# Performance work log

Hardware: AMD Instinct MI355X
Metric: run time of the kernel (lower is better)

The kernel has to match this reference:

```python
import jax, jax.numpy as jnp
import numpy as np

RADIUS = 0.1          # acceptance_radius
CONF = 0.2            # confidence_threshold
MIN_LOCAL = 3         # min_local_correspondences
MIN_GLOBAL = 256      # min_global_correspondences
STEPS = 5             # num_refinement_steps
EPS = 1e-5
NTH = 8               # candidate thresholds CONF - 0.05*k (replaces data-dependent while loop)


def weighted_procrustes(src, tgt, w):
    """Weighted Kabsch. src/tgt: (..., N, 3), w: (..., N). Returns R (...,3,3), t (...,3)."""
    w = w / (jnp.sum(w, axis=-1, keepdims=True) + EPS)
    src_c = jnp.einsum('...n,...nc->...c', w, src)
    tgt_c = jnp.einsum('...n,...nc->...c', w, tgt)
    s0 = src - src_c[..., None, :]
    t0 = tgt - tgt_c[..., None, :]
    H = jnp.einsum('...nc,...n,...nd->...cd', s0, w, t0)  # (...,3,3)
    U, S, Vt = jnp.linalg.svd(H)
    V = jnp.swapaxes(Vt, -1, -2)
    det = jnp.linalg.det(jnp.matmul(V, jnp.swapaxes(U, -1, -2)))
    d = jnp.stack([jnp.ones_like(det), jnp.ones_like(det), det], axis=-1)
    R = jnp.einsum('...ik,...k,...jk->...ij', V, d, U)
    t = tgt_c - jnp.einsum('...ij,...j->...i', R, src_c)
    return R, t


def setup_inputs() -> dict:
    key = jax.random.key(0)
    k0, k1, k2 = jax.random.split(key, 3)
    B, K = 128, 64
    src = jax.random.normal(k0, (B, K, 3), dtype=jnp.float32)
    tgt = jax.random.normal(k1, (B, K, 3), dtype=jnp.float32)
    score_mat = jax.random.normal(k2, (B, K, K), dtype=jnp.float32) * 2.0 - 4.0
    src_masks = jnp.ones((B, K), dtype=bool)
    tgt_masks = jnp.ones((B, K), dtype=bool)
    return {
        'src_knn_points': src,
        'tgt_knn_points': tgt,
        'src_knn_masks': src_masks,
        'tgt_knn_masks': tgt_masks,
        'score_mat': score_mat,
    }


def reference(src_knn_points, tgt_knn_points, src_knn_masks, tgt_knn_masks, score_mat):
    B, K, _ = score_mat.shape
    score = jax.nn.sigmoid(score_mat)
    mask = src_knn_masks[:, :, None] & tgt_knn_masks[:, None, :]  # (B,K,K)

    # --- threshold search (dense replacement for the while loop) ---
    mg = jnp.minimum(min(3 * K, MIN_GLOBAL), jnp.sum(mask))
    th = CONF - 0.05 * jnp.arange(NTH, dtype=score.dtype)
    cnts = jnp.sum((score[None] > th[:, None, None, None]) & mask[None], axis=(1, 2, 3))
    thr = th[jnp.argmax(cnts >= mg)]  # first threshold with enough correspondences

    corr = (score > thr) & mask          # dense corr_mat (B,K,K)
    score = score * corr.astype(score.dtype)

    # --- dense (masked) correspondence batching: all (i,j) pairs per patch ---
    srcP = jnp.broadcast_to(src_knn_points[:, :, None, :], (B, K, K, 3)).reshape(B, K * K, 3)
    tgtP = jnp.broadcast_to(tgt_knn_points[:, None, :, :], (B, K, K, 3)).reshape(B, K * K, 3)
    w = score.reshape(B, K * K)

    # per-patch hypothesis transforms (zero-weight pairs are ignored by Procrustes)
    Rb, tb = weighted_procrustes(srcP, tgtP, w)  # (B,3,3), (B,3)
    counts_b = jnp.sum(corr, axis=(1, 2))
    valid = counts_b >= MIN_LOCAL

    # --- hypothesis verification: inlier counts over all global correspondences ---
    aligned = jnp.einsum('bxy,piy->bpix', Rb, src_knn_points) + tb[:, None, None, :]  # (B,B,K,3)
    cross = jnp.einsum('bpix,pjx->bpij', aligned, tgt_knn_points)                     # (B,B,K,K)
    res2 = (jnp.sum(aligned ** 2, -1)[..., None]
            + jnp.sum(tgt_knn_points ** 2, -1)[None, :, None, :]
            - 2.0 * cross)
    inlier = (res2 < RADIUS ** 2) & corr[None]                                        # (B,B,K,K)
    cnt_T = jnp.where(valid, jnp.sum(inlier, axis=(1, 2, 3)), -1)
    best = jnp.argmax(cnt_T)

    cur = score * inlier[best].astype(score.dtype)

    # --- global refinement ---
    src_all = srcP.reshape(-1, 3)
    tgt_all = tgtP.reshape(-1, 3)
    score_all = score.reshape(-1)
    R, t = weighted_procrustes(src_all, tgt_all, cur.reshape(-1))
    for _ in range(STEPS - 1):
        res = jnp.linalg.norm(tgt_all - (src_all @ R.T + t), axis=-1)
        cur_all = score_all * (res < RADIUS).astype(score.dtype)
        R, t = weighted_procrustes(src_all, tgt_all, cur_all)

    estimated_transform = jnp.eye(4, dtype=score.dtype).at[:3, :3].set(R).at[:3, 3].set(t)
    return estimated_transform, score  # score = dense-masked correspondence scores (B,K,K)
```

## Files before the change

### kernel.cpp

```cpp
#include <hip/hip_runtime.h>
#include <math.h>

#define BB   128
#define KK   64
#define K2   (KK*KK)
#define NTH  8
#define MG   192
#define MIN_LOCAL 3
#define RADIUS2 0.01f
#define RADIUSF 0.1f
#define GRID 256
#define TPB  512
#define NW   8
#define AGT  __HIP_MEMORY_SCOPE_AGENT

static constexpr size_t OFF_ARR   = 0;
static constexpr size_t OFF_MAIL  = 4096;
static constexpr size_t ZERO_BYTES= 8192;
static constexpr size_t OFF_CNT8S = 8192;
static constexpr size_t OFF_CNTB  = 12288;
static constexpr size_t OFF_MSLOT = 28672;
static constexpr size_t OFF_VALID = 45056;
static constexpr size_t OFF_RB    = 45568;
static constexpr size_t OFF_CB    = 51712;

__device__ inline void mail_wait(int* mail, int blk, int ep) {
    int spins = 0;
    unsigned long long t0 = 0;
    while (__hip_atomic_load(&mail[blk * 4], __ATOMIC_RELAXED, AGT) < ep) {
        __builtin_amdgcn_s_sleep(2);
        if ((++spins & 63) == 0) {
            unsigned long long now = __builtin_amdgcn_s_memrealtime();
            if (t0 == 0) t0 = now;
            else if (now - t0 > 10000000ULL) break;
        }
    }
    __atomic_signal_fence(__ATOMIC_SEQ_CST);
}

__device__ inline void sync_point(int* arrived, int* mail, int blk, int lane, int wave,
                                  int ep, int nparts) {
    __syncthreads();
    if (blk == 0) {
        if (wave == 0) {
            if (lane == 0)
                __hip_atomic_store(&arrived[0], ep, __ATOMIC_RELEASE, AGT);
            int spins = 0;
            unsigned long long t0 = 0;
            for (;;) {
                bool ok = true;
                for (int i = lane; i < nparts; i += 64)
                    ok &= (__hip_atomic_load(&arrived[i * 4], __ATOMIC_RELAXED, AGT) >= ep);
                if (__ballot(ok) == ~0ULL) break;
                __builtin_amdgcn_s_sleep(1);
                if ((++spins & 31) == 0) {
                    unsigned long long now = __builtin_amdgcn_s_memrealtime();
                    if (t0 == 0) t0 = now;
                    else if (now - t0 > 10000000ULL) break;
                }
            }
            for (int i = lane; i < GRID; i += 64)
                __hip_atomic_store(&mail[i * 4], ep, __ATOMIC_RELAXED, AGT);
        }
    } else {
        if (lane == 0 && wave == 0) {
            __hip_atomic_store(&arrived[blk * 4], ep, __ATOMIC_RELEASE, AGT);
            mail_wait(mail, blk, ep);
        }
    }
    __atomic_signal_fence(__ATOMIC_SEQ_CST);
    __syncthreads();
}

__device__ inline void eigvec3(const double A[3][3], double lambda, double v[3]) {
    double r0x = A[0][0] - lambda, r0y = A[0][1], r0z = A[0][2];
    double r1x = A[0][1], r1y = A[1][1] - lambda, r1z = A[1][2];
    double r2x = A[0][2], r2y = A[1][2], r2z = A[2][2] - lambda;
    double c0x = r0y * r1z - r0z * r1y, c0y = r0z * r1x - r0x * r1z, c0z = r0x * r1y - r0y * r1x;
    double c1x = r0y * r2z - r0z * r2y, c1y = r0z * r2x - r0x * r2z, c1z = r0x * r2y - r0y * r2x;
    double c2x = r1y * r2z - r1z * r2y, c2y = r1z * r2x - r1x * r2z, c2z = r1x * r2y - r1y * r2x;
    double n0 = c0x * c0x + c0y * c0y + c0z * c0z;
    double n1 = c1x * c1x + c1y * c1y + c1z * c1z;
    double n2 = c2x * c2x + c2y * c2y + c2z * c2z;
    double bx = c0x, by = c0y, bz = c0z, nb = n0;
    if (n1 > nb) { bx = c1x; by = c1y; bz = c1z; nb = n1; }
    if (n2 > nb) { bx = c2x; by = c2y; bz = c2z; nb = n2; }
    if (nb < 1e-280) { v[0] = 1.0; v[1] = 0.0; v[2] = 0.0; return; }
    double s = 1.0 / sqrt(nb);
    v[0] = bx * s; v[1] = by * s; v[2] = bz * s;
}

__device__ inline void eig3(const double A[3][3], double V[3][3], double lam[3]) {
    double q = (A[0][0] + A[1][1] + A[2][2]) / 3.0;
    double a00 = A[0][0] - q, a11 = A[1][1] - q, a22 = A[2][2] - q;
    double p1 = A[0][1] * A[0][1] + A[0][2] * A[0][2] + A[1][2] * A[1][2];
    double p2 = a00 * a00 + a11 * a11 + a22 * a22 + 2.0 * p1;
    if (p2 < 1e-280) {
        lam[0] = q; lam[1] = q; lam[2] = q;
        for (int i = 0; i < 3; i++)
            for (int j = 0; j < 3; j++) V[i][j] = (i == j) ? 1.0 : 0.0;
        return;
    }
    double p = sqrt(p2 / 6.0);
    double ip = 1.0 / p;
    double b00 = a00 * ip, b11 = a11 * ip, b22 = a22 * ip;
    double b01 = A[0][1] * ip, b02 = A[0][2] * ip, b12 = A[1][2] * ip;
    double detB = b00 * (b11 * b22 - b12 * b12)
                - b01 * (b01 * b22 - b12 * b02)
                + b02 * (b01 * b12 - b11 * b02);
    double r = 0.5 * detB;
    r = fmin(1.0, fmax(-1.0, r));
    double phi = acos(r) / 3.0;
    double l0 = q + 2.0 * p * cos(phi);
    double l2 = q + 2.0 * p * cos(phi + 2.0943951023931953);
    double l1 = 3.0 * q - l0 - l2;
    lam[0] = l0; lam[1] = l1; lam[2] = l2;

    double v0[3], v2[3];
    eigvec3(A, l0, v0);
    eigvec3(A, l2, v2);
    double d = v0[0] * v2[0] + v0[1] * v2[1] + v0[2] * v2[2];
    v2[0] -= d * v0[0]; v2[1] -= d * v0[1]; v2[2] -= d * v0[2];
    double n = v2[0] * v2[0] + v2[1] * v2[1] + v2[2] * v2[2];
    if (n < 1e-280) {
        int k = (fabs(v0[0]) <= fabs(v0[1]) && fabs(v0[0]) <= fabs(v0[2])) ? 0
              : ((fabs(v0[1]) <= fabs(v0[2])) ? 1 : 2);
        double ax[3] = {0.0, 0.0, 0.0}; ax[k] = 1.0;
        double dd = v0[k];
        v2[0] = ax[0] - dd * v0[0]; v2[1] = ax[1] - dd * v0[1]; v2[2] = ax[2] - dd * v0[2];
        n = v2[0] * v2[0] + v2[1] * v2[1] + v2[2] * v2[2];
    }
    double s2 = 1.0 / sqrt(n);
    v2[0] *= s2; v2[1] *= s2; v2[2] *= s2;
    double v1[3] = { v2[1] * v0[2] - v2[2] * v0[1],
                     v2[2] * v0[0] - v2[0] * v0[2],
                     v2[0] * v0[1] - v2[1] * v0[0] };
    for (int i = 0; i < 3; i++) { V[i][0] = v0[i]; V[i][1] = v1[i]; V[i][2] = v2[i]; }
}

__device__ inline void kabsch_from_moments(const double* m, double R[3][3], double t[3]) {
    double W = m[0];
    double denom = W + 1e-5;
    double s = W / denom;
    double sc[3], tc[3];
    for (int c = 0; c < 3; c++) { sc[c] = m[1 + c] / denom; tc[c] = m[4 + c] / denom; }
    double H[3][3];
    for (int c = 0; c < 3; c++)
        for (int d = 0; d < 3; d++)
            H[c][d] = m[7 + c * 3 + d] / denom - (2.0 - s) * sc[c] * tc[d];
    double B3[3][3];
    for (int i = 0; i < 3; i++)
        for (int j = 0; j < 3; j++) {
            double v = 0.0;
            for (int k = 0; k < 3; k++) v += H[k][i] * H[k][j];
            B3[i][j] = v;
        }
    double V[3][3], lam[3];
    eig3(B3, V, lam);
    double inv[3];
    for (int k = 0; k < 3; k++) {
        double sg = sqrt(fmax(lam[k], 0.0));
        inv[k] = (sg > 1e-150) ? 1.0 / sg : 0.0;
    }
    double detH = H[0][0] * (H[1][1] * H[2][2] - H[1][2] * H[2][1])
                - H[0][1] * (H[1][0] * H[2][2] - H[1][2] * H[2][0])
                + H[0][2] * (H[1][0] * H[2][1] - H[1][1] * H[2][0]);
    if (detH < 0.0) inv[2] = -inv[2];
    double T2[3][3];
    for (int i = 0; i < 3; i++)
        for (int j = 0; j < 3; j++) {
            double v = 0.0;
            for (int k = 0; k < 3; k++) v += V[i][k] * inv[k] * V[j][k];
            T2[i][j] = v;
        }
    for (int i = 0; i < 3; i++)
        for (int j = 0; j < 3; j++) {
            double v = 0.0;
            for (int k = 0; k < 3; k++) v += T2[i][k] * H[j][k];
            R[i][j] = v;
        }
    for (int i = 0; i < 3; i++) {
        double v = tc[i];
        for (int j = 0; j < 3; j++) v -= R[i][j] * sc[j];
        t[i] = v;
    }
}

__global__ __launch_bounds__(TPB) void k_all(
    const float* __restrict__ src, const float* __restrict__ tgt,
    const float* __restrict__ sm, float* __restrict__ out, char* __restrict__ ws)
{
    int* arrived  = (int*)(ws + OFF_ARR);
    int* mail     = (int*)(ws + OFF_MAIL);
    int* cnt8s    = (int*)(ws + OFF_CNT8S);
    unsigned int* cntB = (unsigned int*)(ws + OFF_CNTB);
    float* mslot  = (float*)(ws + OFF_MSLOT);
    int* validA   = (int*)(ws + OFF_VALID);
    float* Rb     = (float*)(ws + OFF_RB);
    unsigned long long* corrb = (unsigned long long*)(ws + OFF_CB);
    float* score  = out + 16;

    const int t = threadIdx.x, lane = t & 63, wave = t >> 6;
    const int blk = blockIdx.x;

    __shared__ float sScore[4096];
    __shared__ float sS[192];
    __shared__ float sT[256];
    __shared__ float sAl[256];
    __shared__ float sRTall[384];
    __shared__ unsigned long long sCB[64];
    __shared__ float sRed[NW * 16];
    __shared__ int sRedi[NW];
    __shared__ int sCnt[32];
    __shared__ int sC8[NTH];
    __shared__ int sCT[BB], sVv[BB];
    __shared__ int sCTp[512];
    __shared__ double sPartD[512];
    __shared__ double sM[16];
    __shared__ double sRTd[12];
    __shared__ float sRTf[12];
    __shared__ int sBest;
    __shared__ float sThr;

    if (blk < BB) {
        int b = blk;
        float xv[8];
        #pragma unroll
        for (int u = 0; u < 8; u++)
            xv[u] = sm[b * K2 + (u * NW + wave) * KK + lane];
        if (t < 192) sS[t] = src[b * 192 + t];
        if (t < 64) {
            float x = tgt[b * 192 + t * 3], y = tgt[b * 192 + t * 3 + 1], z = tgt[b * 192 + t * 3 + 2];
            sT[t * 4] = x; sT[t * 4 + 1] = y; sT[t * 4 + 2] = z; sT[t * 4 + 3] = x * x + y * y + z * z;
        }
        if (t < NTH) sC8[t] = 0;
        __syncthreads();
        int ck[NTH];
        #pragma unroll
        for (int k = 0; k < NTH; k++) ck[k] = 0;
        for (int u = 0; u < 8; u++) {
            int i = u * NW + wave;
            float s = 1.0f / (1.0f + expf(-xv[u]));
            sScore[i * KK + lane] = s;
            #pragma unroll
            for (int k = 0; k < NTH; k++) {
                unsigned long long bal = __ballot(s > (0.2f - 0.05f * (float)k));
                ck[k] += (int)__popcll(bal);
            }
        }
        if (lane == 0) {
            #pragma unroll
            for (int k = 0; k < NTH; k++) atomicAdd(&sC8[k], ck[k]);
        }
        __syncthreads();
        if (t < NTH)
            __hip_atomic_store(&cnt8s[blk * NTH + t], sC8[t], __ATOMIC_RELAXED, AGT);
        sync_point(arrived, mail, blk, lane, wave, 1, BB);

        if (wave == 0) {
            int k = lane & 7, c = lane >> 3;
            int sct = 0;
            for (int j = 0; j < 16; j++)
                sct += __hip_atomic_load(&cnt8s[(c * 16 + j) * NTH + k], __ATOMIC_RELAXED, AGT);
            sct += __shfl_down(sct, 32);
            sct += __shfl_down(sct, 16);
            sct += __shfl_down(sct, 8);
            unsigned long long bal = __ballot(lane < 8 && sct >= MG);
            if (lane == 0) {
                int kk2 = bal ? (int)__builtin_ctzll(bal) : 0;
                sThr = 0.2f - 0.05f * (float)kk2;
            }
        }
        __syncthreads();

        float thr = sThr;
        float tx0 = sT[lane * 4], ty0 = sT[lane * 4 + 1], tz0 = sT[lane * 4 + 2];
        float acc[16];
        #pragma unroll
        for (int k = 0; k < 16; k++) acc[k] = 0.0f;
        int cnt = 0;
        for (int u = 0; u < 8; u++) {
            int i = u * NW + wave;
            float s = sScore[i * KK + lane];
            bool c = (s > thr);
            float w = c ? s : 0.0f;
            score[b * K2 + i * KK + lane] = w;
            unsigned long long bal = __ballot(c);
            if (lane == 0)
                __hip_atomic_store(&corrb[b * KK + i], bal, __ATOMIC_RELAXED, AGT);
            cnt += c ? 1 : 0;
            float sx = sS[i * 3], sy = sS[i * 3 + 1], sz = sS[i * 3 + 2];
            acc[0]  += w;
            acc[1]  += w * sx; acc[2]  += w * sy; acc[3]  += w * sz;
            acc[4]  += w * tx0; acc[5]  += w * ty0; acc[6]  += w * tz0;
            acc[7]  += w * sx * tx0; acc[8]  += w * sx * ty0; acc[9]  += w * sx * tz0;
            acc[10] += w * sy * tx0; acc[11] += w * sy * ty0; acc[12] += w * sy * tz0;
            acc[13] += w * sz * tx0; acc[14] += w * sz * ty0; acc[15] += w * sz * tz0;
        }
        #pragma unroll
        for (int off = 32; off; off >>= 1) {
            #pragma unroll
            for (int k = 0; k < 16; k++) acc[k] += __shfl_down(acc[k], off);
            cnt += __shfl_down(cnt, off);
        }
        if (lane == 0) {
            for (int k = 0; k < 16; k++) sRed[wave * 16 + k] = acc[k];
            sRedi[wave] = cnt;
        }
        __syncthreads();
        if (t == 0) {
            double m[16];
            for (int k = 0; k < 16; k++) {
                float v = 0.0f;
                for (int wv = 0; wv < NW; wv++) v += sRed[wv * 16 + k];
                m[k] = (double)v;
            }
            double R[3][3], tv[3];
            kabsch_from_moments(m, R, tv);
            for (int i = 0; i < 3; i++)
                for (int j = 0; j < 3; j++)
                    __hip_atomic_store(&Rb[b * 12 + i * 3 + j], (float)R[i][j], __ATOMIC_RELAXED, AGT);
            for (int i = 0; i < 3; i++)
                __hip_atomic_store(&Rb[b * 12 + 9 + i], (float)tv[i], __ATOMIC_RELAXED, AGT);
            int ctot = 0;
            for (int wv = 0; wv < NW; wv++) ctot += sRedi[wv];
            __hip_atomic_store(&validA[b], (ctot >= MIN_LOCAL) ? 1 : 0, __ATOMIC_RELAXED, AGT);
        }
        sync_point(arrived, mail, blk, lane, wave, 2, BB);
    } else {
        if (t == 0) mail_wait(mail, blk, 2);
        __syncthreads();
    }

    if (t < 32) sCnt[t] = 0;
    for (int u = 0; u < 2; u++) {
        int unit = blk + u * GRID;
        int p = unit >> 2, g4 = unit & 3, b0 = g4 * 32;
        __syncthreads();
        if (t < 192) sS[t] = src[p * 192 + t];
        if (t < 64) {
            float x = tgt[p * 192 + t * 3], y = tgt[p * 192 + t * 3 + 1], z = tgt[p * 192 + t * 3 + 2];
            sT[t * 4] = x; sT[t * 4 + 1] = y; sT[t * 4 + 2] = z; sT[t * 4 + 3] = x * x + y * y + z * z;
            sCB[t] = __hip_atomic_load(&corrb[p * KK + t], __ATOMIC_RELAXED, AGT);
        }
        if (t < 384)
            sRTall[t] = __hip_atomic_load(&Rb[b0 * 12 + t], __ATOMIC_RELAXED, AGT);
        __syncthreads();

        int i = t >> 3, jg = t & 7;
        float sx = sS[i * 3], sy = sS[i * 3 + 1], sz = sS[i * 3 + 2];
        unsigned int m8 = (unsigned int)((sCB[i] >> (jg * 8)) & 0xFFULL);
        const float4* sT4 = (const float4*)sT;
        float4 tv0 = sT4[jg * 8 + 0], tv1 = sT4[jg * 8 + 1];
        float4 tv2 = sT4[jg * 8 + 2], tv3 = sT4[jg * 8 + 3];
        float4 tv4 = sT4[jg * 8 + 4], tv5 = sT4[jg * 8 + 5];
        float4 tv6 = sT4[jg * 8 + 6], tv7 = sT4[jg * 8 + 7];

        for (int h = 0; h < 32; h++) {
            const float* RT = &sRTall[h * 12];
            float ax = RT[0] * sx + RT[1] * sy + RT[2] * sz + RT[9];
            float ay = RT[3] * sx + RT[4] * sy + RT[5] * sz + RT[10];
            float az = RT[6] * sx + RT[7] * sy + RT[8] * sz + RT[11];
            float sa = ax * ax + ay * ay + az * az;
            int c = 0;
            #define VCHK(TV, JJ) { \
                float d2 = (sa + TV.w) - 2.0f * (ax * TV.x + ay * TV.y + az * TV.z); \
                c += (d2 < RADIUS2 && ((m8 >> JJ) & 1u)) ? 1 : 0; }
            VCHK(tv0, 0) VCHK(tv1, 1) VCHK(tv2, 2) VCHK(tv3, 3)
            VCHK(tv4, 4) VCHK(tv5, 5) VCHK(tv6, 6) VCHK(tv7, 7)
            #undef VCHK
            #pragma unroll
            for (int off = 32; off; off >>= 1) c += __shfl_down(c, off);
            if (lane == 0) atomicAdd(&sCnt[h], c);
        }
    }
    __syncthreads();
    if (t < 16) {
        unsigned int pk = ((unsigned int)sCnt[2 * t] & 0xFFFFu)
                        | ((unsigned int)sCnt[2 * t + 1] << 16);
        __hip_atomic_store(&cntB[blk * 16 + t], pk, __ATOMIC_RELAXED, AGT);
    }
    if (blk >= BB) {
        __syncthreads();
        if (t == 0) __hip_atomic_store(&arrived[blk * 4], 3, __ATOMIC_RELEASE, AGT);
        return;
    }
    sync_point(arrived, mail, blk, lane, wave, 3, GRID);

    {
        int p = blk;
        if (t < 192) sS[t] = src[p * 192 + t];
        if (t < 64) {
            float x = tgt[p * 192 + t * 3], y = tgt[p * 192 + t * 3 + 1], z = tgt[p * 192 + t * 3 + 2];
            sT[t * 4] = x; sT[t * 4 + 1] = y; sT[t * 4 + 2] = z; sT[t * 4 + 3] = x * x + y * y + z * z;
        }
    }
    {
        int q = t >> 7, h = t & 127;
        int g = h >> 5, r = h & 31, w = r >> 1, sh = (r & 1) * 16;
        int ssum = 0;
        for (int m = q * 16; m < q * 16 + 16; m++) {
            unsigned int wv = __hip_atomic_load(&cntB[((4 * m + g) << 4) + w],
                                                __ATOMIC_RELAXED, AGT);
            ssum += (int)((wv >> sh) & 0xFFFFu);
        }
        sCTp[t] = ssum;
    }
    __syncthreads();
    if (t < BB) {
        sCT[t] = sCTp[t] + sCTp[t + 128] + sCTp[t + 256] + sCTp[t + 384];
        sVv[t] = __hip_atomic_load(&validA[t], __ATOMIC_RELAXED, AGT);
    }
    __syncthreads();
    if (t == 0) {
        int best = 0, bc = -2;
        for (int b = 0; b < BB; b++) {
            int c = sVv[b] ? sCT[b] : -1;
            if (c > bc) { bc = c; best = b; }
        }
        sBest = best;
    }
    __syncthreads();
    if (t < 12)
        sRTd[t] = (double)__hip_atomic_load(&Rb[sBest * 12 + t], __ATOMIC_RELAXED, AGT);
    __syncthreads();

    float thr = sThr;
    for (int it = 0; it < 5; it++) {
        if (t < 12) sRTf[t] = (float)sRTd[t];
        __syncthreads();
        if (t < 64) {
            float x = sS[t * 3], y = sS[t * 3 + 1], z = sS[t * 3 + 2];
            float ax = sRTf[0] * x + sRTf[1] * y + sRTf[2] * z + sRTf[9];
            float ay = sRTf[3] * x + sRTf[4] * y + sRTf[5] * z + sRTf[10];
            float az = sRTf[6] * x + sRTf[7] * y + sRTf[8] * z + sRTf[11];
            sAl[t * 4] = ax; sAl[t * 4 + 1] = ay; sAl[t * 4 + 2] = az;
            sAl[t * 4 + 3] = ax * ax + ay * ay + az * az;
        }
        __syncthreads();
        float tx = sT[lane * 4], ty = sT[lane * 4 + 1], tz = sT[lane * 4 + 2], st2 = sT[lane * 4 + 3];
        float acc[16];
        #pragma unroll
        for (int k = 0; k < 16; k++) acc[k] = 0.0f;
        for (int u = 0; u < 8; u++) {
            int i = u * NW + wave;
            float sx = sS[i * 3], sy = sS[i * 3 + 1], sz = sS[i * 3 + 2];
            float ax = sAl[i * 4], ay = sAl[i * 4 + 1], az = sAl[i * 4 + 2], sa = sAl[i * 4 + 3];
            bool pred;
            if (it == 0) {
                float d2 = (sa + st2) - 2.0f * (ax * tx + ay * ty + az * tz);
                pred = (d2 < RADIUS2);
            } else {
                float dx = tx - ax, dy = ty - ay, dz = tz - az;
                pred = (sqrtf(dx * dx + dy * dy + dz * dz) < RADIUSF);
            }
            float s = sScore[i * KK + lane];
            float w = (s > thr) ? s : 0.0f;
            float wf = pred ? w : 0.0f;
            acc[0]  += wf;
            acc[1]  += wf * sx; acc[2]  += wf * sy; acc[3]  += wf * sz;
            acc[4]  += wf * tx; acc[5]  += wf * ty; acc[6]  += wf * tz;
            acc[7]  += wf * sx * tx; acc[8]  += wf * sx * ty; acc[9]  += wf * sx * tz;
            acc[10] += wf * sy * tx; acc[11] += wf * sy * ty; acc[12] += wf * sy * tz;
            acc[13] += wf * sz * tx; acc[14] += wf * sz * ty; acc[15] += wf * sz * tz;
        }
        #pragma unroll
        for (int off = 32; off; off >>= 1)
            #pragma unroll
            for (int k = 0; k < 16; k++) acc[k] += __shfl_down(acc[k], off);
        if (lane == 0)
            for (int k = 0; k < 16; k++) sRed[wave * 16 + k] = acc[k];
        __syncthreads();
        if (t < 16) {
            float v = 0.0f;
            for (int wv = 0; wv < NW; wv++) v += sRed[wv * 16 + t];
            __hip_atomic_store(&mslot[(((it & 1) * BB + blk) << 4) + t], v,
                               __ATOMIC_RELAXED, AGT);
        }
        if (it < 4) {
            sync_point(arrived, mail, blk, lane, wave, 4 + it, BB);
            {
                int k = t & 15, c = t >> 4;
                double sd = 0.0;
                for (int j = 0; j < 4; j++)
                    sd += (double)__hip_atomic_load(
                        &mslot[(((it & 1) * BB + c * 4 + j) << 4) + k],
                        __ATOMIC_RELAXED, AGT);
                sPartD[t] = sd;
            }
            __syncthreads();
            if (t < 16) {
                double md = 0.0;
                for (int c = 0; c < 32; c++) md += sPartD[c * 16 + t];
                sM[t] = md;
            }
            __syncthreads();
            if (t == 0) {
                double m[16];
                for (int k = 0; k < 16; k++) m[k] = sM[k];
                double R[3][3], tv[3];
                kabsch_from_moments(m, R, tv);
                for (int i = 0; i < 3; i++)
                    for (int j = 0; j < 3; j++) sRTd[i * 3 + j] = R[i][j];
                for (int i = 0; i < 3; i++) sRTd[9 + i] = tv[i];
            }
            __syncthreads();
        } else {
            __syncthreads();
            if (blk != 0) {
                if (t == 0) __hip_atomic_store(&arrived[blk * 4], 8, __ATOMIC_RELEASE, AGT);
                return;
            }
            if (wave == 0) {
                if (lane == 0) __hip_atomic_store(&arrived[0], 8, __ATOMIC_RELEASE, AGT);
                int spins = 0;
                unsigned long long t0 = 0;
                for (;;) {
                    bool ok = true;
                    for (int i = lane; i < BB; i += 64)
                        ok &= (__hip_atomic_load(&arrived[i * 4], __ATOMIC_RELAXED, AGT) >= 8);
                    if (__ballot(ok) == ~0ULL) break;
                    __builtin_amdgcn_s_sleep(1);
                    if ((++spins & 31) == 0) {
                        unsigned long long now = __builtin_amdgcn_s_memrealtime();
                        if (t0 == 0) t0 = now;
                        else if (now - t0 > 10000000ULL) break;
                    }
                }
            }
            __atomic_signal_fence(__ATOMIC_SEQ_CST);
            __syncthreads();
            {
                int k = t & 15, c = t >> 4;
                double sd = 0.0;
                for (int j = 0; j < 4; j++)
                    sd += (double)__hip_atomic_load(&mslot[((c * 4 + j) << 4) + k],
                                                    __ATOMIC_RELAXED, AGT);
                sPartD[t] = sd;
            }
            __syncthreads();
            if (t < 16) {
                double md = 0.0;
                for (int c = 0; c < 32; c++) md += sPartD[c * 16 + t];
                sM[t] = md;
            }
            __syncthreads();
            if (t == 0) {
                double m[16];
                for (int k = 0; k < 16; k++) m[k] = sM[k];
                double R[3][3], tv[3];
                kabsch_from_moments(m, R, tv);
                for (int i = 0; i < 3; i++) {
                    for (int j = 0; j < 3; j++) out[i * 4 + j] = (float)R[i][j];
                    out[i * 4 + 3] = (float)tv[i];
                }
                out[12] = 0.0f; out[13] = 0.0f; out[14] = 0.0f; out[15] = 1.0f;
            }
        }
    }
}

extern "C" void kernel_launch(void* const* d_in, const int* in_sizes, int n_in,
                              void* d_out, int out_size, void* d_ws, size_t ws_size,
                              hipStream_t stream) {
    const float* src = (const float*)d_in[0];
    const float* tgt = (const float*)d_in[1];
    const float* sm  = (const float*)d_in[4];
    float* out = (float*)d_out;
    char* ws = (char*)d_ws;

    hipMemsetAsync(d_ws, 0, ZERO_BYTES, stream);

    k_all<<<GRID, TPB, 0, stream>>>(src, tgt, sm, out, ws);
}
```

Before: 176.9 us.

## Replace grid barriers with per-block tags and single-block reduce-and-publish

Swaps the centralized arrive/mailbox grid barrier for per-block ready tags. Block 0 alone reduces the partial results (threshold counts, best-hypothesis counts, moments), solves Kabsch, and publishes the answer through a small mailbox that the other blocks poll. The verification stage now waits only on the 32 hypothesis blocks and 2 point blocks it actually depends on, instead of the whole grid. This is meant to cut barrier round-trips and the redundant per-block reductions. In exchange, rotation values are published as float rather than double, and the spin loops poll more aggressively.

```diff
diff --git a/kernel.cpp b/kernel.cpp
--- a/kernel.cpp
+++ b/kernel.cpp
@@ -14,21 +14,31 @@
 #define NW   8
 #define AGT  __HIP_MEMORY_SCOPE_AGENT
 
-static constexpr size_t OFF_ARR   = 0;
-static constexpr size_t OFF_MAIL  = 4096;
-static constexpr size_t ZERO_BYTES= 8192;
-static constexpr size_t OFF_CNT8S = 8192;
-static constexpr size_t OFF_CNTB  = 12288;
-static constexpr size_t OFF_MSLOT = 28672;
-static constexpr size_t OFF_VALID = 45056;
-static constexpr size_t OFF_RB    = 45568;
-static constexpr size_t OFF_CB    = 51712;
-
-__device__ inline void mail_wait(int* mail, int blk, int ep) {
+static constexpr size_t OFF_TAGA  = 0;
+static constexpr size_t OFF_TAGB  = 512;
+static constexpr size_t OFF_TAGC  = 1024;
+static constexpr size_t OFF_TAGM  = 2048;
+static constexpr size_t OFF_PUB   = 3072;
+static constexpr size_t ZERO_BYTES= 3328;
+static constexpr size_t OFF_CNT8S = 4096;
+static constexpr size_t OFF_CNTB  = 8192;
+static constexpr size_t OFF_MSLOT = 24576;
+static constexpr size_t OFF_VALID = 40960;
+static constexpr size_t OFF_RB    = 41472;
+static constexpr size_t OFF_CB    = 47616;
+
+#define PUB_THR_TAG 0
+#define PUB_THR_VAL 1
+#define PUB_BEST_TAG 16
+#define PUB_BEST_VAL 17
+#define PUB_R0 32
+#define PUB_R1 48
+
+__device__ inline void wait_ge(int* p, int val) {
     int spins = 0;
     unsigned long long t0 = 0;
-    while (__hip_atomic_load(&mail[blk * 4], __ATOMIC_RELAXED, AGT) < ep) {
-        __builtin_amdgcn_s_sleep(2);
+    while (__hip_atomic_load(p, __ATOMIC_RELAXED, AGT) < val) {
+        if (spins > 8) __builtin_amdgcn_s_sleep(2);
         if ((++spins & 63) == 0) {
             unsigned long long now = __builtin_amdgcn_s_memrealtime();
             if (t0 == 0) t0 = now;
@@ -38,38 +48,61 @@
     __atomic_signal_fence(__ATOMIC_SEQ_CST);
 }
 
-__device__ inline void sync_point(int* arrived, int* mail, int blk, int lane, int wave,
-                                  int ep, int nparts) {
-    __syncthreads();
-    if (blk == 0) {
-        if (wave == 0) {
-            if (lane == 0)
-                __hip_atomic_store(&arrived[0], ep, __ATOMIC_RELEASE, AGT);
-            int spins = 0;
-            unsigned long long t0 = 0;
-            for (;;) {
-                bool ok = true;
-                for (int i = lane; i < nparts; i += 64)
-                    ok &= (__hip_atomic_load(&arrived[i * 4], __ATOMIC_RELAXED, AGT) >= ep);
-                if (__ballot(ok) == ~0ULL) break;
-                __builtin_amdgcn_s_sleep(1);
-                if ((++spins & 31) == 0) {
-                    unsigned long long now = __builtin_amdgcn_s_memrealtime();
-                    if (t0 == 0) t0 = now;
-                    else if (now - t0 > 10000000ULL) break;
-                }
-            }
-            for (int i = lane; i < GRID; i += 64)
-                __hip_atomic_store(&mail[i * 4], ep, __ATOMIC_RELAXED, AGT);
-        }
-    } else {
-        if (lane == 0 && wave == 0) {
-            __hip_atomic_store(&arrived[blk * 4], ep, __ATOMIC_RELEASE, AGT);
-            mail_wait(mail, blk, ep);
+__device__ inline void wait128(const int* tags, int lane, int val) {
+    int spins = 0;
+    unsigned long long t0 = 0;
+    for (;;) {
+        bool ok = (__hip_atomic_load(&tags[lane],      __ATOMIC_RELAXED, AGT) >= val)
+               && (__hip_atomic_load(&tags[lane + 64], __ATOMIC_RELAXED, AGT) >= val);
+        if (__ballot(ok) == ~0ULL) break;
+        if (spins > 16) __builtin_amdgcn_s_sleep(1);
+        if ((++spins & 63) == 0) {
+            unsigned long long now = __builtin_amdgcn_s_memrealtime();
+            if (t0 == 0) t0 = now;
+            else if (__ballot(now - t0 > 10000000ULL) != 0ULL) break;
         }
     }
     __atomic_signal_fence(__ATOMIC_SEQ_CST);
-    __syncthreads();
+}
+
+__device__ inline void wait256(const int* tags, int lane, int val) {
+    int spins = 0;
+    unsigned long long t0 = 0;
+    for (;;) {
+        bool ok = true;
+        #pragma unroll
+        for (int j = 0; j < 4; j++)
+            ok &= (__hip_atomic_load(&tags[lane + j * 64], __ATOMIC_RELAXED, AGT) >= val);
+        if (__ballot(ok) == ~0ULL) break;
+        if (spins > 16) __builtin_amdgcn_s_sleep(1);
+        if ((++spins & 63) == 0) {
+            unsigned long long now = __builtin_amdgcn_s_memrealtime();
+            if (t0 == 0) t0 = now;
+            else if (__ballot(now - t0 > 10000000ULL) != 0ULL) break;
+        }
+    }
+    __atomic_signal_fence(__ATOMIC_SEQ_CST);
+}
+
+__device__ inline void wait_set34(const int* tagB, int lane, int b0, int p0, int p1) {
+    int idx = -1;
+    if (lane < 32) idx = b0 + lane;
+    else if (lane == 32) idx = p0;
+    else if (lane == 33) idx = p1;
+    int spins = 0;
+    unsigned long long t0 = 0;
+    for (;;) {
+        bool ok = (idx < 0) ||
+                  (__hip_atomic_load(&tagB[idx], __ATOMIC_RELAXED, AGT) >= 1);
+        if (__ballot(ok) == ~0ULL) break;
+        if (spins > 8) __builtin_amdgcn_s_sleep(8);
+        if ((++spins & 63) == 0) {
+            unsigned long long now = __builtin_amdgcn_s_memrealtime();
+            if (t0 == 0) t0 = now;
+            else if (__ballot(now - t0 > 10000000ULL) != 0ULL) break;
+        }
+    }
+    __atomic_signal_fence(__ATOMIC_SEQ_CST);
 }
 
 __device__ inline void eigvec3(const double A[3][3], double lambda, double v[3]) {
@@ -190,8 +223,11 @@
     const float* __restrict__ src, const float* __restrict__ tgt,
     const float* __restrict__ sm, float* __restrict__ out, char* __restrict__ ws)
 {
-    int* arrived  = (int*)(ws + OFF_ARR);
-    int* mail     = (int*)(ws + OFF_MAIL);
+    int* tagA     = (int*)(ws + OFF_TAGA);
+    int* tagB     = (int*)(ws + OFF_TAGB);
+    int* tagC     = (int*)(ws + OFF_TAGC);
+    int* tagM     = (int*)(ws + OFF_TAGM);
+    int* pub      = (int*)(ws + OFF_PUB);
     int* cnt8s    = (int*)(ws + OFF_CNT8S);
     unsigned int* cntB = (unsigned int*)(ws + OFF_CNTB);
     float* mslot  = (float*)(ws + OFF_MSLOT);
@@ -215,8 +251,6 @@
     __shared__ int sC8[NTH];
     __shared__ int sCT[BB], sVv[BB];
     __shared__ int sCTp[512];
-    __shared__ double sPartD[512];
-    __shared__ double sM[16];
     __shared__ double sRTd[12];
     __shared__ float sRTf[12];
     __shared__ int sBest;
@@ -255,23 +289,41 @@
         __syncthreads();
         if (t < NTH)
             __hip_atomic_store(&cnt8s[blk * NTH + t], sC8[t], __ATOMIC_RELAXED, AGT);
-        sync_point(arrived, mail, blk, lane, wave, 1, BB);
-
-        if (wave == 0) {
-            int k = lane & 7, c = lane >> 3;
-            int sct = 0;
-            for (int j = 0; j < 16; j++)
-                sct += __hip_atomic_load(&cnt8s[(c * 16 + j) * NTH + k], __ATOMIC_RELAXED, AGT);
-            sct += __shfl_down(sct, 32);
-            sct += __shfl_down(sct, 16);
-            sct += __shfl_down(sct, 8);
-            unsigned long long bal = __ballot(lane < 8 && sct >= MG);
-            if (lane == 0) {
-                int kk2 = bal ? (int)__builtin_ctzll(bal) : 0;
-                sThr = 0.2f - 0.05f * (float)kk2;
-            }
-        }
-        __syncthreads();
+        __syncthreads();
+        if (t == 0)
+            __hip_atomic_store(&tagA[blk], 1, __ATOMIC_RELEASE, AGT);
+
+        if (blk == 0) {
+            if (wave == 0) {
+                wait128(tagA, lane, 1);
+                int a[NTH];
+                #pragma unroll
+                for (int k = 0; k < NTH; k++)
+                    a[k] = __hip_atomic_load(&cnt8s[lane * NTH + k], __ATOMIC_RELAXED, AGT)
+                         + __hip_atomic_load(&cnt8s[(lane + 64) * NTH + k], __ATOMIC_RELAXED, AGT);
+                #pragma unroll
+                for (int off = 32; off; off >>= 1)
+                    #pragma unroll
+                    for (int k = 0; k < NTH; k++) a[k] += __shfl_down(a[k], off);
+                if (lane == 0) {
+                    int kk2 = 0; bool found = false;
+                    #pragma unroll
+                    for (int k = 0; k < NTH; k++)
+                        if (!found && a[k] >= MG) { kk2 = k; found = true; }
+                    float thr = 0.2f - 0.05f * (float)kk2;
+                    __hip_atomic_store(&pub[PUB_THR_VAL], __float_as_int(thr), __ATOMIC_RELAXED, AGT);
+                    __hip_atomic_store(&pub[PUB_THR_TAG], 1, __ATOMIC_RELEASE, AGT);
+                    sThr = thr;
+                }
+            }
+            __syncthreads();
+        } else {
+            if (t == 0) {
+                wait_ge(&pub[PUB_THR_TAG], 1);
+                sThr = __int_as_float(__hip_atomic_load(&pub[PUB_THR_VAL], __ATOMIC_RELAXED, AGT));
+            }
+            __syncthreads();
+        }
 
         float thr = sThr;
         float tx0 = sT[lane * 4], ty0 = sT[lane * 4 + 1], tz0 = sT[lane * 4 + 2];
@@ -326,52 +378,54 @@
             for (int wv = 0; wv < NW; wv++) ctot += sRedi[wv];
             __hip_atomic_store(&validA[b], (ctot >= MIN_LOCAL) ? 1 : 0, __ATOMIC_RELAXED, AGT);
         }
-        sync_point(arrived, mail, blk, lane, wave, 2, BB);
-    } else {
-        if (t == 0) mail_wait(mail, blk, 2);
-        __syncthreads();
-    }
-
-    if (t < 32) sCnt[t] = 0;
-    for (int u = 0; u < 2; u++) {
-        int unit = blk + u * GRID;
-        int p = unit >> 2, g4 = unit & 3, b0 = g4 * 32;
-        __syncthreads();
-        if (t < 192) sS[t] = src[p * 192 + t];
-        if (t < 64) {
-            float x = tgt[p * 192 + t * 3], y = tgt[p * 192 + t * 3 + 1], z = tgt[p * 192 + t * 3 + 2];
-            sT[t * 4] = x; sT[t * 4 + 1] = y; sT[t * 4 + 2] = z; sT[t * 4 + 3] = x * x + y * y + z * z;
-            sCB[t] = __hip_atomic_load(&corrb[p * KK + t], __ATOMIC_RELAXED, AGT);
-        }
-        if (t < 384)
-            sRTall[t] = __hip_atomic_load(&Rb[b0 * 12 + t], __ATOMIC_RELAXED, AGT);
-        __syncthreads();
-
-        int i = t >> 3, jg = t & 7;
-        float sx = sS[i * 3], sy = sS[i * 3 + 1], sz = sS[i * 3 + 2];
-        unsigned int m8 = (unsigned int)((sCB[i] >> (jg * 8)) & 0xFFULL);
-        const float4* sT4 = (const float4*)sT;
-        float4 tv0 = sT4[jg * 8 + 0], tv1 = sT4[jg * 8 + 1];
-        float4 tv2 = sT4[jg * 8 + 2], tv3 = sT4[jg * 8 + 3];
-        float4 tv4 = sT4[jg * 8 + 4], tv5 = sT4[jg * 8 + 5];
-        float4 tv6 = sT4[jg * 8 + 6], tv7 = sT4[jg * 8 + 7];
-
-        for (int h = 0; h < 32; h++) {
-            const float* RT = &sRTall[h * 12];
-            float ax = RT[0] * sx + RT[1] * sy + RT[2] * sz + RT[9];
-            float ay = RT[3] * sx + RT[4] * sy + RT[5] * sz + RT[10];
-            float az = RT[6] * sx + RT[7] * sy + RT[8] * sz + RT[11];
-            float sa = ax * ax + ay * ay + az * az;
-            int c = 0;
-            #define VCHK(TV, JJ) { \
-                float d2 = (sa + TV.w) - 2.0f * (ax * TV.x + ay * TV.y + az * TV.z); \
-                c += (d2 < RADIUS2 && ((m8 >> JJ) & 1u)) ? 1 : 0; }
-            VCHK(tv0, 0) VCHK(tv1, 1) VCHK(tv2, 2) VCHK(tv3, 3)
-            VCHK(tv4, 4) VCHK(tv5, 5) VCHK(tv6, 6) VCHK(tv7, 7)
-            #undef VCHK
-            #pragma unroll
-            for (int off = 32; off; off >>= 1) c += __shfl_down(c, off);
-            if (lane == 0) atomicAdd(&sCnt[h], c);
+        __syncthreads();
+        if (t == 0)
+            __hip_atomic_store(&tagB[blk], 1, __ATOMIC_RELEASE, AGT);
+    }
+
+    {
+        int p0 = blk >> 2, b0 = (blk & 3) * 32;
+        if (wave == 0) wait_set34(tagB, lane, b0, p0, p0 + 64);
+        if (t < 32) sCnt[t] = 0;
+        for (int u = 0; u < 2; u++) {
+            int p = p0 + u * 64;
+            __syncthreads();
+            if (t < 192) sS[t] = src[p * 192 + t];
+            if (t < 64) {
+                float x = tgt[p * 192 + t * 3], y = tgt[p * 192 + t * 3 + 1], z = tgt[p * 192 + t * 3 + 2];
+                sT[t * 4] = x; sT[t * 4 + 1] = y; sT[t * 4 + 2] = z; sT[t * 4 + 3] = x * x + y * y + z * z;
+                sCB[t] = __hip_atomic_load(&corrb[p * KK + t], __ATOMIC_RELAXED, AGT);
+            }
+            if (t < 384)
+                sRTall[t] = __hip_atomic_load(&Rb[b0 * 12 + t], __ATOMIC_RELAXED, AGT);
+            __syncthreads();
+
+            int i = t >> 3, jg = t & 7;
+            float sx = sS[i * 3], sy = sS[i * 3 + 1], sz = sS[i * 3 + 2];
+            unsigned int m8 = (unsigned int)((sCB[i] >> (jg * 8)) & 0xFFULL);
+            const float4* sT4 = (const float4*)sT;
+            float4 tv0 = sT4[jg * 8 + 0], tv1 = sT4[jg * 8 + 1];
+            float4 tv2 = sT4[jg * 8 + 2], tv3 = sT4[jg * 8 + 3];
+            float4 tv4 = sT4[jg * 8 + 4], tv5 = sT4[jg * 8 + 5];
+            float4 tv6 = sT4[jg * 8 + 6], tv7 = sT4[jg * 8 + 7];
+
+            for (int h = 0; h < 32; h++) {
+                const float* RT = &sRTall[h * 12];
+                float ax = RT[0] * sx + RT[1] * sy + RT[2] * sz + RT[9];
+                float ay = RT[3] * sx + RT[4] * sy + RT[5] * sz + RT[10];
+                float az = RT[6] * sx + RT[7] * sy + RT[8] * sz + RT[11];
+                float sa = ax * ax + ay * ay + az * az;
+                int c = 0;
+                #define VCHK(TV, JJ) { \
+                    float d2 = (sa + TV.w) - 2.0f * (ax * TV.x + ay * TV.y + az * TV.z); \
+                    c += (d2 < RADIUS2 && ((m8 >> JJ) & 1u)) ? 1 : 0; }
+                VCHK(tv0, 0) VCHK(tv1, 1) VCHK(tv2, 2) VCHK(tv3, 3)
+                VCHK(tv4, 4) VCHK(tv5, 5) VCHK(tv6, 6) VCHK(tv7, 7)
+                #undef VCHK
+                #pragma unroll
+                for (int off = 32; off; off >>= 1) c += __shfl_down(c, off);
+                if (lane == 0) atomicAdd(&sCnt[h], c);
+            }
         }
     }
     __syncthreads();
@@ -380,47 +434,54 @@
                         | ((unsigned int)sCnt[2 * t + 1] << 16);
         __hip_atomic_store(&cntB[blk * 16 + t], pk, __ATOMIC_RELAXED, AGT);
     }
-    if (blk >= BB) {
-        __syncthreads();
-        if (t == 0) __hip_atomic_store(&arrived[blk * 4], 3, __ATOMIC_RELEASE, AGT);
-        return;
-    }
-    sync_point(arrived, mail, blk, lane, wave, 3, GRID);
-
-    {
-        int p = blk;
-        if (t < 192) sS[t] = src[p * 192 + t];
-        if (t < 64) {
-            float x = tgt[p * 192 + t * 3], y = tgt[p * 192 + t * 3 + 1], z = tgt[p * 192 + t * 3 + 2];
-            sT[t * 4] = x; sT[t * 4 + 1] = y; sT[t * 4 + 2] = z; sT[t * 4 + 3] = x * x + y * y + z * z;
-        }
-    }
-    {
-        int q = t >> 7, h = t & 127;
-        int g = h >> 5, r = h & 31, w = r >> 1, sh = (r & 1) * 16;
-        int ssum = 0;
-        for (int m = q * 16; m < q * 16 + 16; m++) {
-            unsigned int wv = __hip_atomic_load(&cntB[((4 * m + g) << 4) + w],
-                                                __ATOMIC_RELAXED, AGT);
-            ssum += (int)((wv >> sh) & 0xFFFFu);
-        }
-        sCTp[t] = ssum;
-    }
     __syncthreads();
-    if (t < BB) {
-        sCT[t] = sCTp[t] + sCTp[t + 128] + sCTp[t + 256] + sCTp[t + 384];
-        sVv[t] = __hip_atomic_load(&validA[t], __ATOMIC_RELAXED, AGT);
-    }
-    __syncthreads();
-    if (t == 0) {
-        int best = 0, bc = -2;
-        for (int b = 0; b < BB; b++) {
-            int c = sVv[b] ? sCT[b] : -1;
-            if (c > bc) { bc = c; best = b; }
-        }
-        sBest = best;
-    }
-    __syncthreads();
+    if (t == 0)
+        __hip_atomic_store(&tagC[blk], 1, __ATOMIC_RELEASE, AGT);
+    if (blk >= BB) return;
+
+    if (t < 192) sS[t] = src[blk * 192 + t];
+    if (t < 64) {
+        float x = tgt[blk * 192 + t * 3], y = tgt[blk * 192 + t * 3 + 1], z = tgt[blk * 192 + t * 3 + 2];
+        sT[t * 4] = x; sT[t * 4 + 1] = y; sT[t * 4 + 2] = z; sT[t * 4 + 3] = x * x + y * y + z * z;
+    }
+    if (blk == 0) {
+        if (wave == 0) wait256(tagC, lane, 1);
+        __syncthreads();
+        {
+            int q = t >> 7, h = t & 127;
+            int g = h >> 5, r = h & 31, w = r >> 1, sh = (r & 1) * 16;
+            int ssum = 0;
+            for (int m = q * 16; m < q * 16 + 16; m++) {
+                unsigned int wv = __hip_atomic_load(&cntB[((4 * m + g) << 4) + w],
+                                                    __ATOMIC_RELAXED, AGT);
+                ssum += (int)((wv >> sh) & 0xFFFFu);
+            }
+            sCTp[t] = ssum;
+        }
+        __syncthreads();
+        if (t < BB) {
+            sCT[t] = sCTp[t] + sCTp[t + 128] + sCTp[t + 256] + sCTp[t + 384];
+            sVv[t] = __hip_atomic_load(&validA[t], __ATOMIC_RELAXED, AGT);
+        }
+        __syncthreads();
+        if (t == 0) {
+            int best = 0, bc = -2;
+            for (int b = 0; b < BB; b++) {
+                int c = sVv[b] ? sCT[b] : -1;
+                if (c > bc) { bc = c; best = b; }
+            }
+            __hip_atomic_store(&pub[PUB_BEST_VAL], best, __ATOMIC_RELAXED, AGT);
+            __hip_atomic_store(&pub[PUB_BEST_TAG], 1, __ATOMIC_RELEASE, AGT);
+            sBest = best;
+        }
+        __syncthreads();
+    } else {
+        if (t == 0) {
+            wait_ge(&pub[PUB_BEST_TAG], 1);
+            sBest = __hip_atomic_load(&pub[PUB_BEST_VAL], __ATOMIC_RELAXED, AGT);
+        }
+        __syncthreads();
+    }
     if (t < 12)
         sRTd[t] = (double)__hip_atomic_load(&Rb[sBest * 12 + t], __ATOMIC_RELAXED, AGT);
     __syncthreads();
@@ -477,85 +538,78 @@
             __hip_atomic_store(&mslot[(((it & 1) * BB + blk) << 4) + t], v,
                                __ATOMIC_RELAXED, AGT);
         }
+        __syncthreads();
+        if (t == 0)
+            __hip_atomic_store(&tagM[(it & 1) * BB + blk], it + 1, __ATOMIC_RELEASE, AGT);
+
         if (it < 4) {
-            sync_point(arrived, mail, blk, lane, wave, 4 + it, BB);
-            {
-                int k = t & 15, c = t >> 4;
-                double sd = 0.0;
-                for (int j = 0; j < 4; j++)
-                    sd += (double)__hip_atomic_load(
-                        &mslot[(((it & 1) * BB + c * 4 + j) << 4) + k],
-                        __ATOMIC_RELAXED, AGT);
-                sPartD[t] = sd;
-            }
-            __syncthreads();
-            if (t < 16) {
-                double md = 0.0;
-                for (int c = 0; c < 32; c++) md += sPartD[c * 16 + t];
-                sM[t] = md;
-            }
-            __syncthreads();
-            if (t == 0) {
-                double m[16];
-                for (int k = 0; k < 16; k++) m[k] = sM[k];
-                double R[3][3], tv[3];
-                kabsch_from_moments(m, R, tv);
-                for (int i = 0; i < 3; i++)
-                    for (int j = 0; j < 3; j++) sRTd[i * 3 + j] = R[i][j];
-                for (int i = 0; i < 3; i++) sRTd[9 + i] = tv[i];
-            }
-            __syncthreads();
-        } else {
-            __syncthreads();
-            if (blk != 0) {
-                if (t == 0) __hip_atomic_store(&arrived[blk * 4], 8, __ATOMIC_RELEASE, AGT);
-                return;
-            }
-            if (wave == 0) {
-                if (lane == 0) __hip_atomic_store(&arrived[0], 8, __ATOMIC_RELEASE, AGT);
-                int spins = 0;
-                unsigned long long t0 = 0;
-                for (;;) {
-                    bool ok = true;
-                    for (int i = lane; i < BB; i += 64)
-                        ok &= (__hip_atomic_load(&arrived[i * 4], __ATOMIC_RELAXED, AGT) >= 8);
-                    if (__ballot(ok) == ~0ULL) break;
-                    __builtin_amdgcn_s_sleep(1);
-                    if ((++spins & 31) == 0) {
-                        unsigned long long now = __builtin_amdgcn_s_memrealtime();
-                        if (t0 == 0) t0 = now;
-                        else if (now - t0 > 10000000ULL) break;
+            int base = (it & 1) ? PUB_R1 : PUB_R0;
+            if (blk == 0) {
+                if (wave == 0) {
+                    wait128(&tagM[(it & 1) * BB], lane, it + 1);
+                    double a[16];
+                    #pragma unroll
+                    for (int k = 0; k < 16; k++)
+                        a[k] = (double)__hip_atomic_load(
+                                   &mslot[(((it & 1) * BB + lane) << 4) + k], __ATOMIC_RELAXED, AGT)
+                             + (double)__hip_atomic_load(
+                                   &mslot[(((it & 1) * BB + lane + 64) << 4) + k], __ATOMIC_RELAXED, AGT);
+                    #pragma unroll
+                    for (int off = 32; off; off >>= 1)
+                        #pragma unroll
+                        for (int k = 0; k < 16; k++) a[k] += __shfl_down(a[k], off);
+                    if (lane == 0) {
+                        double R[3][3], tv[3];
+                        kabsch_from_moments(a, R, tv);
+                        for (int i = 0; i < 3; i++)
+                            for (int j = 0; j < 3; j++) sRTd[i * 3 + j] = R[i][j];
+                        for (int i = 0; i < 3; i++) sRTd[9 + i] = tv[i];
+                        #pragma unroll
+                        for (int i = 0; i < 3; i++)
+                            for (int j = 0; j < 3; j++)
+                                __hip_atomic_store(&pub[base + 1 + i * 3 + j],
+                                    __float_as_int((float)R[i][j]), __ATOMIC_RELAXED, AGT);
+                        #pragma unroll
+                        for (int i = 0; i < 3; i++)
+                            __hip_atomic_store(&pub[base + 10 + i],
+                                __float_as_int((float)tv[i]), __ATOMIC_RELAXED, AGT);
+                        __hip_atomic_store(&pub[base], it + 1, __ATOMIC_RELEASE, AGT);
                     }
                 }
-            }
-            __atomic_signal_fence(__ATOMIC_SEQ_CST);
-            __syncthreads();
-            {
-                int k = t & 15, c = t >> 4;
-                double sd = 0.0;
-                for (int j = 0; j < 4; j++)
-                    sd += (double)__hip_atomic_load(&mslot[((c * 4 + j) << 4) + k],
-                                                    __ATOMIC_RELAXED, AGT);
-                sPartD[t] = sd;
-            }
-            __syncthreads();
-            if (t < 16) {
-                double md = 0.0;
-                for (int c = 0; c < 32; c++) md += sPartD[c * 16 + t];
-                sM[t] = md;
-            }
-            __syncthreads();
-            if (t == 0) {
-                double m[16];
-                for (int k = 0; k < 16; k++) m[k] = sM[k];
-                double R[3][3], tv[3];
-                kabsch_from_moments(m, R, tv);
-                for (int i = 0; i < 3; i++) {
-                    for (int j = 0; j < 3; j++) out[i * 4 + j] = (float)R[i][j];
-                    out[i * 4 + 3] = (float)tv[i];
+                __syncthreads();
+            } else {
+                if (t == 0) {
+                    wait_ge(&pub[base], it + 1);
+                    for (int i = 0; i < 12; i++)
+                        sRTd[i] = (double)__int_as_float(
+                            __hip_atomic_load(&pub[base + 1 + i], __ATOMIC_RELAXED, AGT));
                 }
-                out[12] = 0.0f; out[13] = 0.0f; out[14] = 0.0f; out[15] = 1.0f;
-            }
+                __syncthreads();
+            }
+        } else {
+            if (blk != 0) return;
+            if (wave == 0) {
+                wait128(&tagM[0], lane, 5);
+                double a[16];
+                #pragma unroll
+                for (int k = 0; k < 16; k++)
+                    a[k] = (double)__hip_atomic_load(&mslot[(lane << 4) + k], __ATOMIC_RELAXED, AGT)
+                         + (double)__hip_atomic_load(&mslot[((lane + 64) << 4) + k], __ATOMIC_RELAXED, AGT);
+                #pragma unroll
+                for (int off = 32; off; off >>= 1)
+                    #pragma unroll
+                    for (int k = 0; k < 16; k++) a[k] += __shfl_down(a[k], off);
+                if (lane == 0) {
+                    double R[3][3], tv[3];
+                    kabsch_from_moments(a, R, tv);
+                    for (int i = 0; i < 3; i++) {
+                        for (int j = 0; j < 3; j++) out[i * 4 + j] = (float)R[i][j];
+                        out[i * 4 + 3] = (float)tv[i];
+                    }
+                    out[12] = 0.0f; out[13] = 0.0f; out[14] = 0.0f; out[15] = 1.0f;
+                }
+            }
+            return;
         }
     }
 }
```

Result: slower. 197.6 us (+11.7%).
